# Kernel optimization log

Hardware: AMD Instinct MI355X
Metric: run time of the kernel (lower is better)

The kernel has to match this reference:

```python
import jax, jax.numpy as jnp
import numpy as np


def setup_inputs() -> dict:
    key = jax.random.key(0)
    B, T = 4096, 2048
    # small positive strains keep C = 2E + I symmetric positive definite
    strain = jax.random.uniform(key, (B, T, 3), dtype=jnp.float32) * 0.2
    ki0 = jnp.float32(1.5)  # learned exponent for order-0 stretch term
    ki1 = jnp.float32(1.0)  # scale on log(J) term (init 1.0 in torch code)
    return {"strain": strain, "ki0": ki0, "ki1": ki1}


def reference(strain, ki0, ki1):
    # Build symmetric 2x2 right Cauchy-Green tensor C = 2E + I implicitly:
    # E00 = s0, E11 = s1, E01 = E10 = 0.5*s2  ->  C01 = s2
    c00 = 2.0 * strain[..., 0] + 1.0          # [B, T]
    c11 = 2.0 * strain[..., 1] + 1.0
    c01 = strain[..., 2]

    det = c00 * c11 - c01 * c01               # det(C)
    J = jnp.sqrt(det)
    log_J = jnp.log(J)

    # closed-form eigenvalues of symmetric 2x2, ascending (matches eigvalsh)
    mean = 0.5 * (c00 + c11)
    rad = jnp.sqrt(0.25 * (c00 - c11) ** 2 + c01 * c01)
    sq_eig = jnp.stack([mean - rad, mean + rad], axis=-1)  # [B, T, 2]

    eig = jnp.sqrt(sq_eig)                    # principal stretches
    aux = J ** (-1.0 / 3.0)                   # volumetric regularizer
    reg_eig = eig * aux[..., None]            # [B, T, 2]

    # order_stretches = 1: one powered-stretch block + scaled log(J)
    kan_input = jnp.concatenate(
        [reg_eig ** ki0, (log_J * ki1)[..., None]], axis=-1
    )                                         # [B, T, 3]
    return kan_input
```

## Files before the change

### kernel.cpp

```cpp
#include <hip/hip_runtime.h>


typedef unsigned int u32;

__device__ __forceinline__ void compute3(float s0, float s1, float s2,
                                         float ki0, float ki1,
                                         float& o0, float& o1, float& o2) {
    const float c00 = __builtin_fmaf(2.0f, s0, 1.0f);
    const float c11 = __builtin_fmaf(2.0f, s1, 1.0f);
    const float c01 = s2;
    const float det = c00 * c11 - c01 * c01;
    const float l2det = __builtin_log2f(det);
    const float mean = 0.5f * (c00 + c11);
    const float diff = 0.5f * (c00 - c11);
    const float rad  = __builtin_sqrtf(__builtin_fmaf(diff, diff, c01 * c01));
    const float l2a = -0.16666666667f * l2det;
    o0 = __builtin_exp2f(ki0 * __builtin_fmaf(0.5f, __builtin_log2f(mean - rad), l2a));
    o1 = __builtin_exp2f(ki0 * __builtin_fmaf(0.5f, __builtin_log2f(mean + rad), l2a));
    o2 = (0.34657359028f * l2det) * ki1;
}

__device__ __forceinline__ float4 process4(float4 v, u32 g, int l, u32 nf4,
                                           float ki0, float ki1,
                                           const float* __restrict__ gf) {
    const u32 r = g % 3u;
    float pw = __shfl_up(v.w, 1);
    float nx = __shfl_down(v.x, 1);

    const bool last  = (l == 63) || (g == nf4 - 1u);
    const bool first = (l == 0);
    float e0 = 0.0f, e1 = 0.0f;
    if (last) {
        if (r == 1u)      nx = gf[(size_t)4 * g + 4];
        else if (r == 0u) { e0 = gf[(size_t)4 * g + 4]; e1 = gf[(size_t)4 * g + 5]; }
    }
    if (first) {
        if (r == 1u)      pw = gf[(size_t)4 * g - 1];
        else if (r == 2u) { e0 = gf[(size_t)4 * g - 2]; e1 = gf[(size_t)4 * g - 1]; }
    }
    const bool fixN = last  && (r == 0u);
    const bool fixP = first && (r == 2u);

    const float pa = (r == 0u) ? v.x : (r == 1u) ? pw  : v.y;
    const float pb = (r == 0u) ? v.y : (r == 1u) ? v.x : v.z;
    const float pc = (r == 0u) ? v.z : (r == 1u) ? v.y : v.w;
    const float sa = fixN ? v.w : fixP ? e0  : v.z;
    const float sb = fixN ? e0  : fixP ? e1  : v.w;
    const float sc = fixN ? e1  : fixP ? v.x : nx;

    float Po0, Po1, Po2, So0, So1, So2;
    compute3(pa, pb, pc, ki0, ki1, Po0, Po1, Po2);
    compute3(sa, sb, sc, ki0, ki1, So0, So1, So2);

    const float nPo0 = __shfl_down(Po0, 1);
    const float pSo2 = __shfl_up(So2, 1);

    float4 o;
    if (r == 0u) {
        o.x = Po0; o.y = Po1; o.z = Po2; o.w = last ? So0 : nPo0;
    } else if (r == 1u) {
        o.x = Po1; o.y = Po2; o.z = So0; o.w = So1;
    } else {
        o.x = fixP ? So2 : pSo2; o.y = Po0; o.z = Po1; o.w = Po2;
    }
    return o;
}

constexpr int TPB = 256;

__global__ __launch_bounds__(TPB) void kan_v7_shfl(
    const float* __restrict__ strain,
    const float* __restrict__ ki0p,
    const float* __restrict__ ki1p,
    float* __restrict__ out,
    int nfloat_i)
{
    const float ki0 = ki0p[0];
    const float ki1 = ki1p[0];
    const u32 nfloat = (u32)nfloat_i;
    const u32 nf4 = nfloat >> 2;
    const u32 t = threadIdx.x;
    const int l = (int)(t & 63u);
    const float4* __restrict__ in4  = (const float4*)strain;
    float4* __restrict__ out4 = (float4*)out;

    const u32 chunk = 2u * (u32)TPB;
    const u32 step = gridDim.x * chunk;
    for (u32 base = blockIdx.x * chunk; base < nf4; base += step) {
        const u32 g0 = base + t;
        const u32 g1 = base + (u32)TPB + t;
        const bool h0 = g0 < nf4;
        const bool h1 = g1 < nf4;
        float4 v0, v1;
        if (h0) v0 = in4[g0];
        if (h1) v1 = in4[g1];
        if (h0) out4[g0] = process4(v0, g0, l, nf4, ki0, ki1, strain);
        if (h1) out4[g1] = process4(v1, g1, l, nf4, ki0, ki1, strain);
    }

    const u32 ntrip = nfloat / 3u;
    const u32 t0 = (nf4 * 4u) / 3u;
    const u32 gs = gridDim.x * (u32)TPB;
    for (u32 e = t0 + blockIdx.x * (u32)TPB + t; e < ntrip; e += gs) {
        float o0, o1, o2;
        compute3(strain[3 * e], strain[3 * e + 1], strain[3 * e + 2],
                 ki0, ki1, o0, o1, o2);
        out[3 * e]     = o0;
        out[3 * e + 1] = o1;
        out[3 * e + 2] = o2;
    }
}

extern "C" void kernel_launch(void* const* d_in, const int* in_sizes, int n_in,
                              void* d_out, int out_size, void* d_ws, size_t ws_size,
                              hipStream_t stream) {
    const float* strain = (const float*)d_in[0];
    const float* ki0p   = (const float*)d_in[1];
    const float* ki1p   = (const float*)d_in[2];
    float* out = (float*)d_out;

    const int nfloat = in_sizes[0];
    const u32 nf4 = ((u32)nfloat) >> 2;
    u32 blocks = (nf4 + 511u) / 512u;
    if (blocks > 4096u) blocks = 4096u;
    if (blocks < 1u) blocks = 1u;

    kan_v7_shfl<<<(int)blocks, TPB, 0, stream>>>(strain, ki0p, ki1p, out, nfloat);
}
```

Before: 180.0 us.

## Stage triplet data through per-wave LDS slabs with register prefetch

Replaces the shuffle-based float4 realignment with per-wave LDS slabs. Each wave loads 192 float4s with coalesced reads, rereads them as 12 contiguous floats per lane to compute four triplets, writes the results back to LDS, then stores them coalesced. It also prefetches the next chunk into registers, cuts one log2 per triplet by using log(lam0)+log(lam1)=log(det), and caps the grid at 2048 blocks. This removes the shuffles, the boundary branches and the extra global reads, in exchange for LDS traffic, possible bank conflicts on the stride-3 float4 accesses, and reliance on wave-only lgkmcnt fences.

```diff
diff --git a/kernel.cpp b/kernel.cpp
--- a/kernel.cpp
+++ b/kernel.cpp
@@ -2,6 +2,8 @@
 
 
 typedef unsigned int u32;
+
+#define WAVE_LDS_FENCE() asm volatile("s_waitcnt lgkmcnt(0)" ::: "memory")
 
 __device__ __forceinline__ void compute3(float s0, float s1, float s2,
                                          float ki0, float ki1,
@@ -14,100 +16,92 @@
     const float mean = 0.5f * (c00 + c11);
     const float diff = 0.5f * (c00 - c11);
     const float rad  = __builtin_sqrtf(__builtin_fmaf(diff, diff, c01 * c01));
+    const float l2lam0 = __builtin_log2f(mean - rad);
     const float l2a = -0.16666666667f * l2det;
-    o0 = __builtin_exp2f(ki0 * __builtin_fmaf(0.5f, __builtin_log2f(mean - rad), l2a));
-    o1 = __builtin_exp2f(ki0 * __builtin_fmaf(0.5f, __builtin_log2f(mean + rad), l2a));
+    o0 = __builtin_exp2f(ki0 * __builtin_fmaf(0.5f, l2lam0, l2a));
+    o1 = __builtin_exp2f(ki0 * __builtin_fmaf(-0.5f, l2lam0,
+                                  __builtin_fmaf(0.5f, l2det, l2a)));
     o2 = (0.34657359028f * l2det) * ki1;
 }
 
-__device__ __forceinline__ float4 process4(float4 v, u32 g, int l, u32 nf4,
-                                           float ki0, float ki1,
-                                           const float* __restrict__ gf) {
-    const u32 r = g % 3u;
-    float pw = __shfl_up(v.w, 1);
-    float nx = __shfl_down(v.x, 1);
+constexpr int TPB = 256;
+constexpr int WPB = TPB / 64;
+constexpr int WCH = 192;
+constexpr int BCH = WPB * WCH;
 
-    const bool last  = (l == 63) || (g == nf4 - 1u);
-    const bool first = (l == 0);
-    float e0 = 0.0f, e1 = 0.0f;
-    if (last) {
-        if (r == 1u)      nx = gf[(size_t)4 * g + 4];
-        else if (r == 0u) { e0 = gf[(size_t)4 * g + 4]; e1 = gf[(size_t)4 * g + 5]; }
-    }
-    if (first) {
-        if (r == 1u)      pw = gf[(size_t)4 * g - 1];
-        else if (r == 2u) { e0 = gf[(size_t)4 * g - 2]; e1 = gf[(size_t)4 * g - 1]; }
-    }
-    const bool fixN = last  && (r == 0u);
-    const bool fixP = first && (r == 2u);
-
-    const float pa = (r == 0u) ? v.x : (r == 1u) ? pw  : v.y;
-    const float pb = (r == 0u) ? v.y : (r == 1u) ? v.x : v.z;
-    const float pc = (r == 0u) ? v.z : (r == 1u) ? v.y : v.w;
-    const float sa = fixN ? v.w : fixP ? e0  : v.z;
-    const float sb = fixN ? e0  : fixP ? e1  : v.w;
-    const float sc = fixN ? e1  : fixP ? v.x : nx;
-
-    float Po0, Po1, Po2, So0, So1, So2;
-    compute3(pa, pb, pc, ki0, ki1, Po0, Po1, Po2);
-    compute3(sa, sb, sc, ki0, ki1, So0, So1, So2);
-
-    const float nPo0 = __shfl_down(Po0, 1);
-    const float pSo2 = __shfl_up(So2, 1);
-
-    float4 o;
-    if (r == 0u) {
-        o.x = Po0; o.y = Po1; o.z = Po2; o.w = last ? So0 : nPo0;
-    } else if (r == 1u) {
-        o.x = Po1; o.y = Po2; o.z = So0; o.w = So1;
-    } else {
-        o.x = fixP ? So2 : pSo2; o.y = Po0; o.z = Po1; o.w = Po2;
-    }
-    return o;
-}
-
-constexpr int TPB = 256;
-
-__global__ __launch_bounds__(TPB) void kan_v7_shfl(
+__global__ __launch_bounds__(TPB) void kan_v9_wavelds(
     const float* __restrict__ strain,
     const float* __restrict__ ki0p,
     const float* __restrict__ ki1p,
     float* __restrict__ out,
     int nfloat_i)
 {
+    __shared__ float4 slab[WPB][WCH];
     const float ki0 = ki0p[0];
     const float ki1 = ki1p[0];
     const u32 nfloat = (u32)nfloat_i;
     const u32 nf4 = nfloat >> 2;
+    const u32 nchunk = nf4 / BCH;
     const u32 t = threadIdx.x;
-    const int l = (int)(t & 63u);
-    const float4* __restrict__ in4  = (const float4*)strain;
+    const u32 w = t >> 6;
+    const u32 l = t & 63u;
+    float4* S = slab[w];
+    const float4* __restrict__ in4 = (const float4*)strain;
     float4* __restrict__ out4 = (float4*)out;
+    const u32 G = gridDim.x;
 
-    const u32 chunk = 2u * (u32)TPB;
-    const u32 step = gridDim.x * chunk;
-    for (u32 base = blockIdx.x * chunk; base < nf4; base += step) {
-        const u32 g0 = base + t;
-        const u32 g1 = base + (u32)TPB + t;
-        const bool h0 = g0 < nf4;
-        const bool h1 = g1 < nf4;
-        float4 v0, v1;
-        if (h0) v0 = in4[g0];
-        if (h1) v1 = in4[g1];
-        if (h0) out4[g0] = process4(v0, g0, l, nf4, ki0, ki1, strain);
-        if (h1) out4[g1] = process4(v1, g1, l, nf4, ki0, ki1, strain);
+    u32 c = blockIdx.x;
+    float4 p0, p1, p2;
+    if (c < nchunk) {
+        const float4* b = in4 + (size_t)c * BCH + w * WCH;
+        p0 = b[l]; p1 = b[l + 64]; p2 = b[l + 128];
+    }
+    while (c < nchunk) {
+        S[l] = p0; S[l + 64] = p1; S[l + 128] = p2;
+
+        const u32 cn = c + G;
+        if (cn < nchunk) {
+            const float4* b = in4 + (size_t)cn * BCH + w * WCH;
+            p0 = b[l]; p1 = b[l + 64]; p2 = b[l + 128];
+        }
+
+        WAVE_LDS_FENCE();
+
+        const float4 a  = S[3u * l];
+        const float4 b4 = S[3u * l + 1];
+        const float4 c4 = S[3u * l + 2];
+
+        float o0,o1,o2,o3,o4,o5,o6,o7,o8,o9,oa,ob;
+        compute3(a.x,  a.y,  a.z,  ki0, ki1, o0, o1, o2);
+        compute3(a.w,  b4.x, b4.y, ki0, ki1, o3, o4, o5);
+        compute3(b4.z, b4.w, c4.x, ki0, ki1, o6, o7, o8);
+        compute3(c4.y, c4.z, c4.w, ki0, ki1, o9, oa, ob);
+
+        S[3u * l]     = make_float4(o0, o1, o2, o3);
+        S[3u * l + 1] = make_float4(o4, o5, o6, o7);
+        S[3u * l + 2] = make_float4(o8, o9, oa, ob);
+
+        WAVE_LDS_FENCE();
+
+        const float4 q0 = S[l], q1 = S[l + 64], q2 = S[l + 128];
+        float4* ob4 = out4 + (size_t)c * BCH + w * WCH;
+        ob4[l] = q0; ob4[l + 64] = q1; ob4[l + 128] = q2;
+
+        WAVE_LDS_FENCE();
+
+        c = cn;
     }
 
     const u32 ntrip = nfloat / 3u;
-    const u32 t0 = (nf4 * 4u) / 3u;
-    const u32 gs = gridDim.x * (u32)TPB;
+    const u32 t0 = nchunk * (BCH * 4u / 3u);
+    const u32 gs = G * (u32)TPB;
     for (u32 e = t0 + blockIdx.x * (u32)TPB + t; e < ntrip; e += gs) {
-        float o0, o1, o2;
+        float x0, x1, x2;
         compute3(strain[3 * e], strain[3 * e + 1], strain[3 * e + 2],
-                 ki0, ki1, o0, o1, o2);
-        out[3 * e]     = o0;
-        out[3 * e + 1] = o1;
-        out[3 * e + 2] = o2;
+                 ki0, ki1, x0, x1, x2);
+        out[3 * e]     = x0;
+        out[3 * e + 1] = x1;
+        out[3 * e + 2] = x2;
     }
 }
 
@@ -121,9 +115,9 @@
 
     const int nfloat = in_sizes[0];
     const u32 nf4 = ((u32)nfloat) >> 2;
-    u32 blocks = (nf4 + 511u) / 512u;
-    if (blocks > 4096u) blocks = 4096u;
+    u32 blocks = nf4 / (u32)BCH;
+    if (blocks > 2048u) blocks = 2048u;
     if (blocks < 1u) blocks = 1u;
 
-    kan_v7_shfl<<<(int)blocks, TPB, 0, stream>>>(strain, ki0p, ki1p, out, nfloat);
+    kan_v9_wavelds<<<(int)blocks, TPB, 0, stream>>>(strain, ki0p, ki1p, out, nfloat);
 }
```

Result: no change. 179.5 us (-0.3%).
